# Kernel tuning notes

Hardware: AMD Instinct MI355X
Metric: run time of the kernel (lower is better)

## Reference

```python
import jax, jax.numpy as jnp
import numpy as np

# Constant from livnium.kernel.constants (assumed scalar; value taken as 1.0).
K_O = 1.0
EPS = 1e-12  # F.normalize default eps

B, D, C = 16384, 1024, 3
F_DIM = D + 10  # features = h_final (D) + 10 scalar features


def setup_inputs() -> dict:
    key = jax.random.key(0)
    ks = jax.random.split(key, 8)
    s1 = 1.0 / np.sqrt(F_DIM)
    return {
        "h_final": jax.random.normal(ks[0], (B, D), jnp.float32),
        "v_p": jax.random.normal(ks[1], (B, D), jnp.float32),
        "v_h": jax.random.normal(ks[2], (B, D), jnp.float32),
        "neutral_dir": jax.random.normal(ks[3], (D,), jnp.float32),
        "neutral_scale": jnp.array(1.0, jnp.float32),
        "w1": jax.random.normal(ks[4], (F_DIM, F_DIM), jnp.float32) * s1,
        "b1": jnp.zeros((F_DIM,), jnp.float32),
        "w2": jax.random.normal(ks[5], (C, F_DIM), jnp.float32) * s1,
        "b2": jnp.zeros((C,), jnp.float32),
    }


def _normalize(x, axis):
    n = jnp.linalg.norm(x, axis=axis, keepdims=True)
    return x / jnp.maximum(n, EPS)


def reference(h_final, v_p, v_h, neutral_dir, neutral_scale, w1, b1, w2, b2):
    v_p_n = _normalize(v_p, -1)                      # [B, D]
    v_h_n = _normalize(v_h, -1)                      # [B, D]
    nd_n = _normalize(neutral_dir, 0)                # [D]

    # alignment(): cosine of the unit vectors == batched dot product.
    align = jnp.sum(v_p_n * v_h_n, axis=-1, keepdims=True)        # [B, 1]
    opp = jnp.sum(-v_p_n * v_h_n, axis=-1, keepdims=True)          # [B, 1]
    align_neutral_p = neutral_scale * jnp.sum(v_p_n * nd_n, axis=-1, keepdims=True)
    align_neutral_h = neutral_scale * jnp.sum(v_h_n * nd_n, axis=-1, keepdims=True)

    energy = K_O * ((1.0 + align) * 0.5)
    expose_neg = (1.0 - align) * 0.5
    dist_p_h = jnp.linalg.norm(v_h - v_p, axis=-1, keepdims=True)
    r_p = jnp.linalg.norm(v_p, axis=-1, keepdims=True)
    r_h = jnp.linalg.norm(v_h, axis=-1, keepdims=True)
    r_final = jnp.linalg.norm(h_final, axis=-1, keepdims=True)

    features = jnp.concatenate(
        [h_final, align, opp, energy, expose_neg, dist_p_h,
         r_p, r_h, r_final, align_neutral_p, align_neutral_h], axis=-1)  # [B, D+10]

    hidden = jax.nn.relu(features @ w1.T + b1)
    logits = hidden @ w2.T + b2                      # [B, C]
    return logits
```

## Files before the change

### kernel.cpp

```cpp
#include <hip/hip_runtime.h>
#include <cstdint>
#include <cstddef>

#define B_ROWS 16384
#define D_DIM  1024
#define F_REAL 1034
#define N_PAD  1152
#define K_PAD  1056
#define EPSN   1e-12f

typedef __bf16 bf16x8 __attribute__((ext_vector_type(8)));
typedef float  f32x4  __attribute__((ext_vector_type(4)));

__device__ __forceinline__ unsigned short f2bf(float f) {
    __bf16 b = (__bf16)f;
    return __builtin_bit_cast(unsigned short, b);
}

__global__ __launch_bounds__(256)
void prep_kernel(const float* __restrict__ h, const float* __restrict__ vp,
                 const float* __restrict__ vh, const float* __restrict__ nd,
                 const float* __restrict__ nsp, unsigned short* __restrict__ A)
{
    const int b = blockIdx.x;
    const int t = threadIdx.x;
    const float4* hp  = (const float4*)(h  + (size_t)b * D_DIM);
    const float4* vpp = (const float4*)(vp + (size_t)b * D_DIM);
    const float4* vhp = (const float4*)(vh + (size_t)b * D_DIM);
    const float4* ndp = (const float4*)nd;

    float4 p = vpp[t], q = vhp[t], f = hp[t], n = ndp[t];

    float s_pp = p.x*p.x + p.y*p.y + p.z*p.z + p.w*p.w;
    float s_hh = q.x*q.x + q.y*q.y + q.z*q.z + q.w*q.w;
    float s_pv = p.x*q.x + p.y*q.y + p.z*q.z + p.w*q.w;
    float s_ff = f.x*f.x + f.y*f.y + f.z*f.z + f.w*f.w;
    float dx = q.x-p.x, dy = q.y-p.y, dz = q.z-p.z, dw = q.w-p.w;
    float s_dd = dx*dx + dy*dy + dz*dz + dw*dw;
    float s_pn = p.x*n.x + p.y*n.y + p.z*n.z + p.w*n.w;
    float s_hn = q.x*n.x + q.y*n.y + q.z*n.z + q.w*n.w;
    float s_nn = n.x*n.x + n.y*n.y + n.z*n.z + n.w*n.w;

    ushort4 ho;
    ho.x = f2bf(f.x); ho.y = f2bf(f.y); ho.z = f2bf(f.z); ho.w = f2bf(f.w);
    *(ushort4*)(A + (size_t)b * K_PAD + t * 4) = ho;

    #pragma unroll
    for (int m = 32; m >= 1; m >>= 1) {
        s_pp += __shfl_xor(s_pp, m, 64);
        s_hh += __shfl_xor(s_hh, m, 64);
        s_pv += __shfl_xor(s_pv, m, 64);
        s_ff += __shfl_xor(s_ff, m, 64);
        s_dd += __shfl_xor(s_dd, m, 64);
        s_pn += __shfl_xor(s_pn, m, 64);
        s_hn += __shfl_xor(s_hn, m, 64);
        s_nn += __shfl_xor(s_nn, m, 64);
    }
    __shared__ float red[4][8];
    const int w = t >> 6;
    if ((t & 63) == 0) {
        red[w][0] = s_pp; red[w][1] = s_hh; red[w][2] = s_pv; red[w][3] = s_ff;
        red[w][4] = s_dd; red[w][5] = s_pn; red[w][6] = s_hn; red[w][7] = s_nn;
    }
    __syncthreads();
    if (t == 0) {
        float v[8];
        #pragma unroll
        for (int i = 0; i < 8; ++i)
            v[i] = red[0][i] + red[1][i] + red[2][i] + red[3][i];
        float np_ = sqrtf(v[0]), nh_ = sqrtf(v[1]), nf = sqrtf(v[3]);
        float nn_ = sqrtf(v[7]);
        float npc = fmaxf(np_, EPSN), nhc = fmaxf(nh_, EPSN), nnc = fmaxf(nn_, EPSN);
        float align = v[2] / (npc * nhc);
        float ns = nsp[0];
        float feat[10];
        feat[0] = align;
        feat[1] = -align;
        feat[2] = 0.5f * (1.0f + align);
        feat[3] = 0.5f * (1.0f - align);
        feat[4] = sqrtf(v[4]);
        feat[5] = np_;
        feat[6] = nh_;
        feat[7] = nf;
        feat[8] = ns * v[5] / (npc * nnc);
        feat[9] = ns * v[6] / (nhc * nnc);
        unsigned short* dst = A + (size_t)b * K_PAD + D_DIM;
        #pragma unroll
        for (int i = 0; i < 10; ++i) dst[i] = f2bf(feat[i]);
        #pragma unroll
        for (int i = 10; i < 32; ++i) dst[i] = 0;
    }
}

__global__ __launch_bounds__(256)
void convw_kernel(const float* __restrict__ w1, unsigned short* __restrict__ Bm)
{
    const int i = blockIdx.x;
    for (int j = threadIdx.x; j < K_PAD; j += 256) {
        float v = (i < F_REAL && j < F_REAL) ? w1[(size_t)i * F_REAL + j] : 0.0f;
        Bm[(size_t)i * K_PAD + j] = f2bf(v);
    }
}

__global__ __launch_bounds__(256)
void initout_kernel(const float* __restrict__ b2, float* __restrict__ out)
{
    int i = blockIdx.x * 256 + threadIdx.x;
    if (i < B_ROWS * 3) out[i] = b2[i % 3];
}

#define GLDS(g, l) __builtin_amdgcn_global_load_lds(                          \
        (const __attribute__((address_space(1))) void*)(g),                   \
        (__attribute__((address_space(3))) void*)(l), 16, 0, 0)

__global__ __launch_bounds__(256)
void gemm_kernel(const unsigned short* __restrict__ A,
                 const unsigned short* __restrict__ Bm,
                 const float* __restrict__ b1, const float* __restrict__ w2,
                 float* __restrict__ out)
{
    __shared__ __bf16 As[128 * 32];
    __shared__ __bf16 Bs[128 * 32];

    const int tid  = threadIdx.x;
    const int lane = tid & 63;
    const int wave = tid >> 6;
    const int wm = wave >> 1, wn = wave & 1;
    const int bm = blockIdx.x, bn = blockIdx.y;

    const unsigned short* ga[4];
    __bf16* la[4];
    #pragma unroll
    for (int o = 0; o < 2; ++o) {
        int s   = o * 256 + tid;
        int row = s >> 2;
        int kc  = (s & 3) ^ (row & 3);
        ga[o]     = A  + (size_t)(bm * 128 + row) * K_PAD + kc * 8;
        la[o]     = As + s * 8;
        ga[o + 2] = Bm + (size_t)(bn * 128 + row) * K_PAD + kc * 8;
        la[o + 2] = Bs + s * 8;
    }

    const int col  = lane & 15;
    const int quad = lane >> 4;
    const int swz  = quad ^ (col & 3);
    int aoff[4], boff[4];
    #pragma unroll
    for (int i = 0; i < 4; ++i) {
        aoff[i] = ((wm * 64 + i * 16 + col) * 4 + swz) * 8;
        boff[i] = ((wn * 64 + i * 16 + col) * 4 + swz) * 8;
    }

    f32x4 acc[4][4];
    #pragma unroll
    for (int i = 0; i < 4; ++i)
        #pragma unroll
        for (int j = 0; j < 4; ++j)
            acc[i][j] = (f32x4){0.f, 0.f, 0.f, 0.f};

    for (int kt = 0; kt < K_PAD / 32; ++kt) {
        if (kt) __syncthreads();
        #pragma unroll
        for (int o = 0; o < 4; ++o)
            GLDS(ga[o] + kt * 32, la[o]);
        __syncthreads();

        bf16x8 av[4], bv[4];
        #pragma unroll
        for (int i = 0; i < 4; ++i) av[i] = *(const bf16x8*)(As + aoff[i]);
        #pragma unroll
        for (int i = 0; i < 4; ++i) bv[i] = *(const bf16x8*)(Bs + boff[i]);
        #pragma unroll
        for (int i = 0; i < 4; ++i)
            #pragma unroll
            for (int j = 0; j < 4; ++j)
                acc[i][j] = __builtin_amdgcn_mfma_f32_16x16x32_bf16(
                                av[i], bv[j], acc[i][j], 0, 0, 0);
    }

    float bias[4], w20[4], w21[4], w22[4];
    #pragma unroll
    for (int ni = 0; ni < 4; ++ni) {
        int n = bn * 128 + wn * 64 + ni * 16 + col;
        bool v = n < F_REAL;
        bias[ni] = v ? b1[n] : 0.0f;
        w20[ni]  = v ? w2[n] : 0.0f;
        w21[ni]  = v ? w2[F_REAL + n] : 0.0f;
        w22[ni]  = v ? w2[2 * F_REAL + n] : 0.0f;
    }
    #pragma unroll
    for (int mi = 0; mi < 4; ++mi) {
        float c0[4] = {0,0,0,0}, c1[4] = {0,0,0,0}, c2[4] = {0,0,0,0};
        #pragma unroll
        for (int ni = 0; ni < 4; ++ni) {
            #pragma unroll
            for (int r = 0; r < 4; ++r) {
                float hd = fmaxf(acc[mi][ni][r] + bias[ni], 0.0f);
                c0[r] += hd * w20[ni];
                c1[r] += hd * w21[ni];
                c2[r] += hd * w22[ni];
            }
        }
        #pragma unroll
        for (int m = 8; m >= 1; m >>= 1) {
            #pragma unroll
            for (int r = 0; r < 4; ++r) {
                c0[r] += __shfl_xor(c0[r], m, 64);
                c1[r] += __shfl_xor(c1[r], m, 64);
                c2[r] += __shfl_xor(c2[r], m, 64);
            }
        }
        if (col == 0) {
            int gm = bm * 128 + wm * 64 + mi * 16 + quad * 4;
            #pragma unroll
            for (int r = 0; r < 4; ++r) {
                atomicAdd(out + (size_t)(gm + r) * 3 + 0, c0[r]);
                atomicAdd(out + (size_t)(gm + r) * 3 + 1, c1[r]);
                atomicAdd(out + (size_t)(gm + r) * 3 + 2, c2[r]);
            }
        }
    }
}

extern "C" void kernel_launch(void* const* d_in, const int* in_sizes, int n_in,
                              void* d_out, int out_size, void* d_ws, size_t ws_size,
                              hipStream_t stream)
{
    const float* h  = (const float*)d_in[0];
    const float* vp = (const float*)d_in[1];
    const float* vh = (const float*)d_in[2];
    const float* nd = (const float*)d_in[3];
    const float* ns = (const float*)d_in[4];
    const float* w1 = (const float*)d_in[5];
    const float* b1 = (const float*)d_in[6];
    const float* w2 = (const float*)d_in[7];
    const float* b2 = (const float*)d_in[8];
    float* out = (float*)d_out;

    unsigned short* Afull = (unsigned short*)d_ws;
    unsigned short* Bfull = Afull + (size_t)B_ROWS * K_PAD;

    prep_kernel<<<B_ROWS, 256, 0, stream>>>(h, vp, vh, nd, ns, Afull);
    convw_kernel<<<N_PAD, 256, 0, stream>>>(w1, Bfull);
    initout_kernel<<<(B_ROWS * 3 + 255) / 256, 256, 0, stream>>>(b2, out);
    gemm_kernel<<<dim3(B_ROWS / 128, N_PAD / 128), 256, 0, stream>>>(
        Afull, Bfull, b1, w2, out);
}
```

Before: 308.4 us.

## Double-buffer GEMM LDS tiles and process one row per wave in prep

The GEMM kernel now keeps two LDS buffers for the A and B tiles. It issues the global-to-LDS load for the next K tile before the MFMA work on the current tile, so memory latency can overlap compute, and one barrier per iteration is removed. The prep kernel now assigns one row per 64-lane wave, with each lane handling four float4 chunks, so the shared-memory cross-wave reduction and block barrier go away. The cost is twice the LDS footprint in the GEMM, which may lower occupancy, and more serial work per lane in prep.

```diff
diff --git a/kernel.cpp b/kernel.cpp
--- a/kernel.cpp
+++ b/kernel.cpp
@@ -7,6 +7,7 @@
 #define F_REAL 1034
 #define N_PAD  1152
 #define K_PAD  1056
+#define NK     (K_PAD / 32)
 #define EPSN   1e-12f
 
 typedef __bf16 bf16x8 __attribute__((ext_vector_type(8)));
@@ -22,28 +23,36 @@
                  const float* __restrict__ vh, const float* __restrict__ nd,
                  const float* __restrict__ nsp, unsigned short* __restrict__ A)
 {
-    const int b = blockIdx.x;
-    const int t = threadIdx.x;
-    const float4* hp  = (const float4*)(h  + (size_t)b * D_DIM);
-    const float4* vpp = (const float4*)(vp + (size_t)b * D_DIM);
-    const float4* vhp = (const float4*)(vh + (size_t)b * D_DIM);
+    const int row  = blockIdx.x * 4 + (threadIdx.x >> 6);
+    const int lane = threadIdx.x & 63;
+    const float4* hp  = (const float4*)(h  + (size_t)row * D_DIM);
+    const float4* vpp = (const float4*)(vp + (size_t)row * D_DIM);
+    const float4* vhp = (const float4*)(vh + (size_t)row * D_DIM);
     const float4* ndp = (const float4*)nd;
-
-    float4 p = vpp[t], q = vhp[t], f = hp[t], n = ndp[t];
-
-    float s_pp = p.x*p.x + p.y*p.y + p.z*p.z + p.w*p.w;
-    float s_hh = q.x*q.x + q.y*q.y + q.z*q.z + q.w*q.w;
-    float s_pv = p.x*q.x + p.y*q.y + p.z*q.z + p.w*q.w;
-    float s_ff = f.x*f.x + f.y*f.y + f.z*f.z + f.w*f.w;
-    float dx = q.x-p.x, dy = q.y-p.y, dz = q.z-p.z, dw = q.w-p.w;
-    float s_dd = dx*dx + dy*dy + dz*dz + dw*dw;
-    float s_pn = p.x*n.x + p.y*n.y + p.z*n.z + p.w*n.w;
-    float s_hn = q.x*n.x + q.y*n.y + q.z*n.z + q.w*n.w;
-    float s_nn = n.x*n.x + n.y*n.y + n.z*n.z + n.w*n.w;
-
-    ushort4 ho;
-    ho.x = f2bf(f.x); ho.y = f2bf(f.y); ho.z = f2bf(f.z); ho.w = f2bf(f.w);
-    *(ushort4*)(A + (size_t)b * K_PAD + t * 4) = ho;
+    unsigned short* arow = A + (size_t)row * K_PAD;
+
+    float s_pp = 0.f, s_hh = 0.f, s_pv = 0.f, s_ff = 0.f;
+    float s_dd = 0.f, s_pn = 0.f, s_hn = 0.f, s_nn = 0.f;
+
+    #pragma unroll
+    for (int c = 0; c < 4; ++c) {
+        const int idx = lane + c * 64;
+        float4 p = vpp[idx], q = vhp[idx], f = hp[idx], n = ndp[idx];
+
+        s_pp += p.x*p.x + p.y*p.y + p.z*p.z + p.w*p.w;
+        s_hh += q.x*q.x + q.y*q.y + q.z*q.z + q.w*q.w;
+        s_pv += p.x*q.x + p.y*q.y + p.z*q.z + p.w*q.w;
+        s_ff += f.x*f.x + f.y*f.y + f.z*f.z + f.w*f.w;
+        float dx = q.x-p.x, dy = q.y-p.y, dz = q.z-p.z, dw = q.w-p.w;
+        s_dd += dx*dx + dy*dy + dz*dz + dw*dw;
+        s_pn += p.x*n.x + p.y*n.y + p.z*n.z + p.w*n.w;
+        s_hn += q.x*n.x + q.y*n.y + q.z*n.z + q.w*n.w;
+        s_nn += n.x*n.x + n.y*n.y + n.z*n.z + n.w*n.w;
+
+        ushort4 ho;
+        ho.x = f2bf(f.x); ho.y = f2bf(f.y); ho.z = f2bf(f.z); ho.w = f2bf(f.w);
+        *(ushort4*)(arow + idx * 4) = ho;
+    }
 
     #pragma unroll
     for (int m = 32; m >= 1; m >>= 1) {
@@ -56,39 +65,29 @@
         s_hn += __shfl_xor(s_hn, m, 64);
         s_nn += __shfl_xor(s_nn, m, 64);
     }
-    __shared__ float red[4][8];
-    const int w = t >> 6;
-    if ((t & 63) == 0) {
-        red[w][0] = s_pp; red[w][1] = s_hh; red[w][2] = s_pv; red[w][3] = s_ff;
-        red[w][4] = s_dd; red[w][5] = s_pn; red[w][6] = s_hn; red[w][7] = s_nn;
-    }
-    __syncthreads();
-    if (t == 0) {
-        float v[8];
+
+    if (lane == 0) {
+        float np_ = sqrtf(s_pp), nh_ = sqrtf(s_hh), nf = sqrtf(s_ff);
+        float npc = fmaxf(np_, EPSN), nhc = fmaxf(nh_, EPSN);
+        float nnc = fmaxf(sqrtf(s_nn), EPSN);
+        float align = s_pv / (npc * nhc);
+        float ns = nsp[0];
+        unsigned short fo[32];
+        fo[0] = f2bf(align);
+        fo[1] = f2bf(-align);
+        fo[2] = f2bf(0.5f * (1.0f + align));
+        fo[3] = f2bf(0.5f * (1.0f - align));
+        fo[4] = f2bf(sqrtf(s_dd));
+        fo[5] = f2bf(np_);
+        fo[6] = f2bf(nh_);
+        fo[7] = f2bf(nf);
+        fo[8] = f2bf(ns * s_pn / (npc * nnc));
+        fo[9] = f2bf(ns * s_hn / (nhc * nnc));
+        #pragma unroll
+        for (int i = 10; i < 32; ++i) fo[i] = 0;
         #pragma unroll
         for (int i = 0; i < 8; ++i)
-            v[i] = red[0][i] + red[1][i] + red[2][i] + red[3][i];
-        float np_ = sqrtf(v[0]), nh_ = sqrtf(v[1]), nf = sqrtf(v[3]);
-        float nn_ = sqrtf(v[7]);
-        float npc = fmaxf(np_, EPSN), nhc = fmaxf(nh_, EPSN), nnc = fmaxf(nn_, EPSN);
-        float align = v[2] / (npc * nhc);
-        float ns = nsp[0];
-        float feat[10];
-        feat[0] = align;
-        feat[1] = -align;
-        feat[2] = 0.5f * (1.0f + align);
-        feat[3] = 0.5f * (1.0f - align);
-        feat[4] = sqrtf(v[4]);
-        feat[5] = np_;
-        feat[6] = nh_;
-        feat[7] = nf;
-        feat[8] = ns * v[5] / (npc * nnc);
-        feat[9] = ns * v[6] / (nhc * nnc);
-        unsigned short* dst = A + (size_t)b * K_PAD + D_DIM;
-        #pragma unroll
-        for (int i = 0; i < 10; ++i) dst[i] = f2bf(feat[i]);
-        #pragma unroll
-        for (int i = 10; i < 32; ++i) dst[i] = 0;
+            *(ushort4*)(arow + D_DIM + i * 4) = *(ushort4*)(fo + i * 4);
     }
 }
 
@@ -119,8 +118,8 @@
                  const float* __restrict__ b1, const float* __restrict__ w2,
                  float* __restrict__ out)
 {
-    __shared__ __bf16 As[128 * 32];
-    __shared__ __bf16 Bs[128 * 32];
+    __shared__ __bf16 As[2][128 * 32];
+    __shared__ __bf16 Bs[2][128 * 32];
 
     const int tid  = threadIdx.x;
     const int lane = tid & 63;
@@ -129,16 +128,19 @@
     const int bm = blockIdx.x, bn = blockIdx.y;
 
     const unsigned short* ga[4];
-    __bf16* la[4];
+    __bf16* l0[4];
+    __bf16* l1[4];
     #pragma unroll
     for (int o = 0; o < 2; ++o) {
         int s   = o * 256 + tid;
         int row = s >> 2;
         int kc  = (s & 3) ^ (row & 3);
         ga[o]     = A  + (size_t)(bm * 128 + row) * K_PAD + kc * 8;
-        la[o]     = As + s * 8;
+        l0[o]     = &As[0][s * 8];
+        l1[o]     = &As[1][s * 8];
         ga[o + 2] = Bm + (size_t)(bn * 128 + row) * K_PAD + kc * 8;
-        la[o + 2] = Bs + s * 8;
+        l0[o + 2] = &Bs[0][s * 8];
+        l1[o + 2] = &Bs[1][s * 8];
     }
 
     const int col  = lane & 15;
@@ -158,18 +160,26 @@
         for (int j = 0; j < 4; ++j)
             acc[i][j] = (f32x4){0.f, 0.f, 0.f, 0.f};
 
-    for (int kt = 0; kt < K_PAD / 32; ++kt) {
-        if (kt) __syncthreads();
-        #pragma unroll
-        for (int o = 0; o < 4; ++o)
-            GLDS(ga[o] + kt * 32, la[o]);
+    #pragma unroll
+    for (int o = 0; o < 4; ++o)
+        GLDS(ga[o], l0[o]);
+
+    for (int kt = 0; kt < NK; ++kt) {
         __syncthreads();
+        if (kt + 1 < NK) {
+            __bf16** ln = ((kt + 1) & 1) ? l1 : l0;
+            #pragma unroll
+            for (int o = 0; o < 4; ++o)
+                GLDS(ga[o] + (kt + 1) * 32, ln[o]);
+        }
+        const __bf16* Ab = As[kt & 1];
+        const __bf16* Bb = Bs[kt & 1];
 
         bf16x8 av[4], bv[4];
         #pragma unroll
-        for (int i = 0; i < 4; ++i) av[i] = *(const bf16x8*)(As + aoff[i]);
-        #pragma unroll
-        for (int i = 0; i < 4; ++i) bv[i] = *(const bf16x8*)(Bs + boff[i]);
+        for (int i = 0; i < 4; ++i) av[i] = *(const bf16x8*)(Ab + aoff[i]);
+        #pragma unroll
+        for (int i = 0; i < 4; ++i) bv[i] = *(const bf16x8*)(Bb + boff[i]);
         #pragma unroll
         for (int i = 0; i < 4; ++i)
             #pragma unroll
@@ -240,7 +250,7 @@
     unsigned short* Afull = (unsigned short*)d_ws;
     unsigned short* Bfull = Afull + (size_t)B_ROWS * K_PAD;
 
-    prep_kernel<<<B_ROWS, 256, 0, stream>>>(h, vp, vh, nd, ns, Afull);
+    prep_kernel<<<B_ROWS / 4, 256, 0, stream>>>(h, vp, vh, nd, ns, Afull);
     convw_kernel<<<N_PAD, 256, 0, stream>>>(w1, Bfull);
     initout_kernel<<<(B_ROWS * 3 + 255) / 256, 256, 0, stream>>>(b2, out);
     gemm_kernel<<<dim3(B_ROWS / 128, N_PAD / 128), 256, 0, stream>>>(
```

Measured after the change: 343.4 us. 1.11x slower.
